# Performance work log

Measured on AMD Instinct MI355X. Metric: run time of the kernel, lower is better.

Reference implementation:

```python
import jax, jax.numpy as jnp
import numpy as np

DIM = 192
HEADS = 8
EPS = 1e-12

def conv2d(x, w, groups=1, padding='SAME'):
    return jax.lax.conv_general_dilated(
        x, w, window_strides=(1, 1), padding=padding,
        dimension_numbers=('NCHW', 'OIHW', 'NCHW'),
        feature_group_count=groups)

def setup_inputs() -> dict:
    key = jax.random.key(0)
    ks = jax.random.split(key, 6)
    b, c, h, w = 8, DIM, 128, 128
    x = jax.random.normal(ks[0], (b, c, h, w), dtype=jnp.float32)
    # depthwise 3x3 conv on x (groups=dim): OIHW with I=1
    w_dw = jax.random.normal(ks[1], (DIM, 1, 3, 3), dtype=jnp.float32) * 0.1
    # 1x1 qkv projection
    w_qkv = jax.random.normal(ks[2], (DIM * 3, DIM, 1, 1), dtype=jnp.float32) * (1.0 / np.sqrt(DIM))
    # depthwise 3x3 on qkv (groups=3*dim)
    w_qkvdw = jax.random.normal(ks[3], (DIM * 3, 1, 3, 3), dtype=jnp.float32) * 0.1
    # 1x1 output projection
    w_proj = jax.random.normal(ks[4], (DIM, DIM, 1, 1), dtype=jnp.float32) * (1.0 / np.sqrt(DIM))
    temperature = jnp.ones((HEADS, 1, 1), dtype=jnp.float32)
    rescale = jnp.ones((HEADS, 1), dtype=jnp.float32)
    return {"x": x, "w_dw": w_dw, "w_qkv": w_qkv, "w_qkvdw": w_qkvdw,
            "w_proj": w_proj, "temperature": temperature, "rescale": rescale}

def l2norm_lastdim(t):
    # matches F.normalize(t, dim=-1, eps=1e-12)
    n = jnp.sqrt(jnp.sum(t * t, axis=-1, keepdims=True))
    return t / jnp.maximum(n, EPS)

def reference(x, w_dw, w_qkv, w_qkvdw, w_proj, temperature, rescale):
    b, c, h, w = x.shape
    heads = HEADS
    c_head = c // heads
    # variance (unbiased, like torch.var default) of depthwise-conv features over H,W
    xd = conv2d(x, w_dw, groups=c)                      # [b,c,h,w]
    var = jnp.var(xd, axis=(-2, -1), ddof=1)            # [b,c]
    var = var.reshape(b, heads, c_head)                 # [b,head,c_head]
    # qkv: 1x1 conv then depthwise 3x3
    qkv = conv2d(conv2d(x, w_qkv), w_qkvdw, groups=3 * c)  # [b,3c,h,w]
    q, k, v = jnp.split(qkv, 3, axis=1)
    def to_heads(t):
        return t.reshape(b, heads, c_head, h * w)       # b head c (h w)
    q, k, v = to_heads(q), to_heads(k), to_heads(v)
    q = l2norm_lastdim(q)
    k = l2norm_lastdim(k)
    # channel attention: [b,head,c_head,c_head]
    attn = jnp.einsum('bhcn,bhdn->bhcd', q, k) * temperature
    # diagonal bias from variance, scaled per-head
    diag = rescale * var                                # [b,head,c_head]
    attn = attn + jnp.einsum('bhc,cd->bhcd', diag, jnp.eye(c_head, dtype=attn.dtype))
    attn = jax.nn.softmax(attn, axis=-1)
    out = jnp.einsum('bhcd,bhdn->bhcn', attn, v)        # [b,head,c_head,hw]
    out = out.reshape(b, c, h, w)
    return conv2d(out, w_proj)
```

## Files before the change

kernel.cpp:

```cpp
#include <hip/hip_runtime.h>
#include <hip/hip_bf16.h>

typedef unsigned short ushort_t;
typedef __bf16 bf16x8 __attribute__((ext_vector_type(8)));
typedef float f32x4 __attribute__((ext_vector_type(4)));
typedef unsigned short us8 __attribute__((ext_vector_type(8)));
typedef unsigned short us4 __attribute__((ext_vector_type(4)));

#define HW 16384
#define CDIM 192
#define QKVC 576

static __device__ __forceinline__ float b2f(unsigned short u) {
    union { unsigned int i; float f; } cv; cv.i = ((unsigned int)u) << 16; return cv.f;
}
static __device__ __forceinline__ unsigned short f2b(float f) {
    union { __bf16 h; unsigned short u; } cv; cv.h = (__bf16)f; return cv.u;
}

__global__ __launch_bounds__(256) void k_cvt(const float* __restrict__ src,
                                             ushort_t* __restrict__ dst, int n8) {
    int i = blockIdx.x * 256 + threadIdx.x;
    if (i >= n8) return;
    f32x4 a = *(const f32x4*)&src[i * 8];
    f32x4 b = *(const f32x4*)&src[i * 8 + 4];
    us8 o;
#pragma unroll
    for (int e = 0; e < 4; ++e) { o[e] = f2b(a[e]); o[4 + e] = f2b(b[e]); }
    *(us8*)&dst[i * 8] = o;
}

__global__ __launch_bounds__(256) void k_dwvar(const float* __restrict__ x,
                                               const float* __restrict__ wdw,
                                               float* __restrict__ var,
                                               ushort_t* __restrict__ xb) {
    __shared__ __align__(16) float pl[128 * 132 + 132];
    __shared__ float red[8];
    int bc = blockIdx.x;
    int c = bc % CDIM;
    const float* xp = x + (size_t)bc * HW;
    ushort_t* xbp = xb + (size_t)bc * HW;
    int t = threadIdx.x;
#pragma unroll
    for (int i = 0; i < 16; ++i) {
        int gi = t + i * 256;
        int y = gi >> 5, xq = (gi & 31) << 2;
        f32x4 v4 = *(const f32x4*)&xp[gi * 4];
        *(f32x4*)&pl[y * 132 + xq] = v4;
        us4 b4;
#pragma unroll
        for (int j = 0; j < 4; ++j) b4[j] = f2b(v4[j]);
        *(us4*)&xbp[gi * 4] = b4;
    }
    if (t < 33) { f32x4 zz = {0.f, 0.f, 0.f, 0.f}; *(f32x4*)&pl[16896 + t * 4] = zz; }
    float w[9];
#pragma unroll
    for (int j = 0; j < 9; ++j) w[j] = wdw[c * 9 + j];
    __syncthreads();

    int y = t >> 1, xs = (t & 1) * 64;
    int yb0 = (y > 0)   ? (y - 1) * 132 : 16896;
    int yb1 = y * 132;
    int yb2 = (y < 127) ? (y + 1) * 132 : 16896;
    float l0 = 0.f, l1 = 0.f, l2 = 0.f;
    if (xs != 0) { l0 = pl[yb0 + 63]; l1 = pl[yb1 + 63]; l2 = pl[yb2 + 63]; }
    float s1 = 0.f, s2 = 0.f;
#pragma unroll
    for (int g = 0; g < 8; ++g) {
        int x0 = xs + g * 8;
        float e0[10], e1[10], e2[10];
        e0[0] = l0; e1[0] = l1; e2[0] = l2;
        f32x4 a0 = *(const f32x4*)&pl[yb0 + x0], b0 = *(const f32x4*)&pl[yb0 + x0 + 4];
        f32x4 a1 = *(const f32x4*)&pl[yb1 + x0], b1 = *(const f32x4*)&pl[yb1 + x0 + 4];
        f32x4 a2 = *(const f32x4*)&pl[yb2 + x0], b2 = *(const f32x4*)&pl[yb2 + x0 + 4];
#pragma unroll
        for (int j = 0; j < 4; ++j) {
            e0[1 + j] = a0[j]; e0[5 + j] = b0[j];
            e1[1 + j] = a1[j]; e1[5 + j] = b1[j];
            e2[1 + j] = a2[j]; e2[5 + j] = b2[j];
        }
        float r0 = 0.f, r1 = 0.f, r2 = 0.f;
        if (x0 + 8 < 128) { r0 = pl[yb0 + x0 + 8]; r1 = pl[yb1 + x0 + 8]; r2 = pl[yb2 + x0 + 8]; }
        e0[9] = r0; e1[9] = r1; e2[9] = r2;
#pragma unroll
        for (int j = 0; j < 8; ++j) {
            float o = e0[j] * w[0] + e0[j + 1] * w[1] + e0[j + 2] * w[2]
                    + e1[j] * w[3] + e1[j + 1] * w[4] + e1[j + 2] * w[5]
                    + e2[j] * w[6] + e2[j + 1] * w[7] + e2[j + 2] * w[8];
            s1 += o; s2 += o * o;
        }
        l0 = e0[8]; l1 = e1[8]; l2 = e2[8];
    }
#pragma unroll
    for (int off = 32; off; off >>= 1) { s1 += __shfl_xor(s1, off); s2 += __shfl_xor(s2, off); }
    int wv = t >> 6;
    if ((t & 63) == 0) { red[wv * 2] = s1; red[wv * 2 + 1] = s2; }
    __syncthreads();
    if (t == 0) {
        float S1 = red[0] + red[2] + red[4] + red[6];
        float S2 = red[1] + red[3] + red[5] + red[7];
        var[bc] = (S2 - S1 * S1 * (1.0f / 16384.f)) * (1.0f / 16383.f);
    }
}

__global__ __launch_bounds__(256) void k_dwqkv(const ushort_t* __restrict__ qkvraw,
                                               const float* __restrict__ wqd,
                                               ushort_t* __restrict__ qkvd,
                                               float* __restrict__ ssq) {
    __shared__ __align__(16) ushort_t pl[128 * 136 + 136];
    __shared__ float red[4];
    int bo = blockIdx.x;
    int o = bo % QKVC, b = bo / QKVC;
    const ushort_t* xp = qkvraw + (size_t)bo * HW;
    ushort_t* op = qkvd + (size_t)bo * HW;
    int t = threadIdx.x;
#pragma unroll
    for (int i = 0; i < 8; ++i) {
        int gi = t + i * 256;
        int y = gi >> 4, xo = (gi & 15) * 8;
        *(us8*)&pl[y * 136 + xo] = *(const us8*)&xp[gi * 8];
    }
    if (t < 17) { us8 zz = {}; *(us8*)&pl[17408 + t * 8] = zz; }
    float w[9];
#pragma unroll
    for (int j = 0; j < 9; ++j) w[j] = wqd[o * 9 + j];
    __syncthreads();

    int y = t >> 1, xs = (t & 1) * 64;
    int yb0 = (y > 0)   ? (y - 1) * 136 : 17408;
    int yb1 = y * 136;
    int yb2 = (y < 127) ? (y + 1) * 136 : 17408;
    float l0 = 0.f, l1 = 0.f, l2 = 0.f;
    if (xs != 0) { l0 = b2f(pl[yb0 + 63]); l1 = b2f(pl[yb1 + 63]); l2 = b2f(pl[yb2 + 63]); }
    float s2 = 0.f;
#pragma unroll
    for (int g = 0; g < 8; ++g) {
        int x0 = xs + g * 8;
        us8 v0 = *(const us8*)&pl[yb0 + x0];
        us8 v1 = *(const us8*)&pl[yb1 + x0];
        us8 v2 = *(const us8*)&pl[yb2 + x0];
        float r0 = 0.f, r1 = 0.f, r2 = 0.f;
        if (x0 + 8 < 128) { r0 = b2f(pl[yb0 + x0 + 8]); r1 = b2f(pl[yb1 + x0 + 8]); r2 = b2f(pl[yb2 + x0 + 8]); }
        float e0[10], e1[10], e2[10];
        e0[0] = l0; e1[0] = l1; e2[0] = l2;
#pragma unroll
        for (int j = 0; j < 8; ++j) { e0[j + 1] = b2f(v0[j]); e1[j + 1] = b2f(v1[j]); e2[j + 1] = b2f(v2[j]); }
        e0[9] = r0; e1[9] = r1; e2[9] = r2;
        us8 ob;
#pragma unroll
        for (int j = 0; j < 8; ++j) {
            float ov = e0[j] * w[0] + e0[j + 1] * w[1] + e0[j + 2] * w[2]
                     + e1[j] * w[3] + e1[j + 1] * w[4] + e1[j + 2] * w[5]
                     + e2[j] * w[6] + e2[j + 1] * w[7] + e2[j + 2] * w[8];
            unsigned short bits = f2b(ov);
            ob[j] = bits;
            float rv = b2f(bits);
            s2 += rv * rv;
        }
        *(us8*)&op[(size_t)y * 128 + x0] = ob;
        l0 = e0[8]; l1 = e1[8]; l2 = e2[8];
    }
    if (o < 2 * CDIM) {
#pragma unroll
        for (int off = 32; off; off >>= 1) s2 += __shfl_xor(s2, off);
        int wv = t >> 6;
        if ((t & 63) == 0) red[wv] = s2;
        __syncthreads();
        if (t == 0) ssq[b * 384 + o] = red[0] + red[1] + red[2] + red[3];
    }
}

template<int CF>
__global__ __launch_bounds__(256) void k_gemm(const ushort_t* __restrict__ Av, long sAb,
                                              const ushort_t* __restrict__ Bv, long sBb,
                                              void* __restrict__ Cv, long sCb, int K) {
    __shared__ __align__(16) char smem[49152];
    ushort_t* As = (ushort_t*)smem;
    ushort_t* Bs = (ushort_t*)(smem + 24576);
    int t = threadIdx.x;
    int wv = t >> 6, lane = t & 63, quad = lane >> 4, l15 = lane & 15;
    size_t aoff = (size_t)blockIdx.z * sAb + (size_t)blockIdx.y * 192 * K;
    size_t boff = (size_t)blockIdx.z * sBb + (size_t)blockIdx.x * 128;
    size_t coff = (size_t)blockIdx.z * sCb + (size_t)blockIdx.y * 192 * HW + (size_t)blockIdx.x * 128;
    f32x4 acc[24] = {};
    int bkr = t >> 3, bn0 = (t & 7) * 16, tlow = t & 7;
    int gk0 = bkr >> 3, klo = bkr & 7;
    const ushort_t* Bp = Bv + boff;
    us8 pb0 = *(const us8*)&Bp[(size_t)bkr * HW + bn0];
    us8 pb1 = *(const us8*)&Bp[(size_t)bkr * HW + bn0 + 8];
    us8 pb2 = *(const us8*)&Bp[(size_t)(bkr + 32) * HW + bn0];
    us8 pb3 = *(const us8*)&Bp[(size_t)(bkr + 32) * HW + bn0 + 8];
    int nIter = K >> 6;
    for (int it = 0; it < nIter; ++it) {
        int kk = it << 6;
#pragma unroll
        for (int i = 0; i < 6; ++i) {
            int s = t + i * 256;
            int row = s >> 3, kc = (s & 7) * 8;
            int kcs = kc ^ ((row & 7) * 8);
            *(uint4*)&As[row * 64 + kcs] = *(const uint4*)&Av[aoff + (size_t)row * K + kk + kc];
        }
#pragma unroll
        for (int e = 0; e < 8; ++e) {
            int col0 = ((gk0 ^ tlow ^ e) << 3) + klo;
            Bs[(bn0 + e) * 64 + col0] = pb0[e];
            Bs[(bn0 + 8 + e) * 64 + col0] = pb1[e];
            int col1 = (((gk0 + 4) ^ tlow ^ e) << 3) + klo;
            Bs[(bn0 + e) * 64 + col1] = pb2[e];
            Bs[(bn0 + 8 + e) * 64 + col1] = pb3[e];
        }
        __syncthreads();
        if (it + 1 < nIter) {
            const ushort_t* Bn = &Bp[(size_t)(kk + 64) * HW];
            pb0 = *(const us8*)&Bn[(size_t)bkr * HW + bn0];
            pb1 = *(const us8*)&Bn[(size_t)bkr * HW + bn0 + 8];
            pb2 = *(const us8*)&Bn[(size_t)(bkr + 32) * HW + bn0];
            pb3 = *(const us8*)&Bn[(size_t)(bkr + 32) * HW + bn0 + 8];
        }
#pragma unroll
        for (int s = 0; s < 2; ++s) {
            int r0 = wv * 16 + l15, r1 = 64 + r0, r2 = 128 + r0;
            int ko = s * 32 + quad * 8;
            bf16x8 af0 = *(const bf16x8*)&As[r0 * 64 + (ko ^ ((r0 & 7) * 8))];
            bf16x8 af1 = *(const bf16x8*)&As[r1 * 64 + (ko ^ ((r1 & 7) * 8))];
            bf16x8 af2 = *(const bf16x8*)&As[r2 * 64 + (ko ^ ((r2 & 7) * 8))];
#pragma unroll
            for (int tc = 0; tc < 8; ++tc) {
                int n = tc * 16 + l15;
                int g = (s * 4 + quad) ^ ((tc ^ l15) & 7);
                bf16x8 bfr = *(const bf16x8*)&Bs[n * 64 + (g << 3)];
                acc[tc]      = __builtin_amdgcn_mfma_f32_16x16x32_bf16(af0, bfr, acc[tc],      0, 0, 0);
                acc[8 + tc]  = __builtin_amdgcn_mfma_f32_16x16x32_bf16(af1, bfr, acc[8 + tc],  0, 0, 0);
                acc[16 + tc] = __builtin_amdgcn_mfma_f32_16x16x32_bf16(af2, bfr, acc[16 + tc], 0, 0, 0);
            }
        }
        __syncthreads();
    }
    if (CF == 0) {
        ushort_t* Ct = (ushort_t*)smem;
#pragma unroll
        for (int rt = 0; rt < 3; ++rt)
#pragma unroll
            for (int tc = 0; tc < 8; ++tc)
#pragma unroll
                for (int r = 0; r < 4; ++r)
                    Ct[(rt * 64 + wv * 16 + quad * 4 + r) * 128 + tc * 16 + l15] = f2b(acc[rt * 8 + tc][r]);
        __syncthreads();
        ushort_t* Co = (ushort_t*)Cv;
#pragma unroll
        for (int i = 0; i < 12; ++i) {
            int s = t + i * 256;
            int row = s >> 4, c8 = (s & 15) * 8;
            *(us8*)&Co[coff + (size_t)row * HW + c8] = *(us8*)&Ct[row * 128 + c8];
        }
    } else {
        float* Cf = (float*)smem;
        float* Co = (float*)Cv;
#pragma unroll
        for (int rt = 0; rt < 3; ++rt) {
            if (rt) __syncthreads();
#pragma unroll
            for (int tc = 0; tc < 8; ++tc)
#pragma unroll
                for (int r = 0; r < 4; ++r)
                    Cf[(wv * 16 + quad * 4 + r) * 128 + tc * 16 + l15] = acc[rt * 8 + tc][r];
            __syncthreads();
#pragma unroll
            for (int i = 0; i < 8; ++i) {
                int s = t + i * 256;
                int row = s >> 5, c4 = (s & 31) * 4;
                *(f32x4*)&Co[coff + (size_t)(rt * 64 + row) * HW + c4] = *(f32x4*)&Cf[row * 128 + c4];
            }
        }
    }
}

__global__ __launch_bounds__(256) void k_gram(const ushort_t* __restrict__ qkvd,
                                              float* __restrict__ G) {
    __shared__ __align__(16) ushort_t qs[24 * 264];
    __shared__ __align__(16) ushort_t ks[24 * 264];
    int bh = blockIdx.y;
    int b = bh >> 3, h = bh & 7;
    int t = threadIdx.x, wv = t >> 6, lane = t & 63, quad = lane >> 4, l15 = lane & 15;
    const ushort_t* qb = qkvd + (size_t)b * 9437184 + (size_t)(h * 24) * HW;
    const ushort_t* kp = qb + (size_t)CDIM * HW;
    f32x4 a00 = {}, a01 = {}, a10 = {}, a11 = {};
    bf16x8 z = {};
    bool hi = (l15 < 8);
    int kbase0 = blockIdx.x * 2048;
    for (int sub = 0; sub < 8; ++sub) {
        int kbase = kbase0 + sub * 256;
#pragma unroll
        for (int j = 0; j < 3; ++j) {
            int gi = t + j * 256;
            int row = gi >> 5, c8 = (gi & 31) * 8;
            *(us8*)&qs[row * 264 + c8] = *(const us8*)&qb[(size_t)row * HW + kbase + c8];
            *(us8*)&ks[row * 264 + c8] = *(const us8*)&kp[(size_t)row * HW + kbase + c8];
        }
        __syncthreads();
#pragma unroll
        for (int s = 0; s < 2; ++s) {
            int ko = (wv * 2 + s) * 32 + quad * 8;
            bf16x8 qa0 = *(const bf16x8*)&qs[l15 * 264 + ko];
            bf16x8 qa1 = hi ? *(const bf16x8*)&qs[(16 + l15) * 264 + ko] : z;
            bf16x8 kb0 = *(const bf16x8*)&ks[l15 * 264 + ko];
            bf16x8 kb1 = hi ? *(const bf16x8*)&ks[(16 + l15) * 264 + ko] : z;
            a00 = __builtin_amdgcn_mfma_f32_16x16x32_bf16(qa0, kb0, a00, 0, 0, 0);
            a01 = __builtin_amdgcn_mfma_f32_16x16x32_bf16(qa0, kb1, a01, 0, 0, 0);
            a10 = __builtin_amdgcn_mfma_f32_16x16x32_bf16(qa1, kb0, a10, 0, 0, 0);
            a11 = __builtin_amdgcn_mfma_f32_16x16x32_bf16(qa1, kb1, a11, 0, 0, 0);
        }
        __syncthreads();
    }
    float* Gp = G + (size_t)bh * 576;
#pragma unroll
    for (int r = 0; r < 4; ++r) {
        int r0 = quad * 4 + r, r1 = 16 + quad * 4 + r;
        int c0 = l15, c1 = 16 + l15;
        atomicAdd(&Gp[r0 * 24 + c0], a00[r]);
        if (c1 < 24) atomicAdd(&Gp[r0 * 24 + c1], a01[r]);
        if (r1 < 24) atomicAdd(&Gp[r1 * 24 + c0], a10[r]);
        if (r1 < 24 && c1 < 24) atomicAdd(&Gp[r1 * 24 + c1], a11[r]);
    }
}

__global__ __launch_bounds__(256) void k_smweff(const float* __restrict__ G,
                                                const float* __restrict__ ssq,
                                                const float* __restrict__ var,
                                                const float* __restrict__ wproj,
                                                const float* __restrict__ temp,
                                                const float* __restrict__ resc,
                                                ushort_t* __restrict__ Weff) {
    int b = blockIdx.x, t = threadIdx.x;
    __shared__ float P[8 * 24 * 24];
    __shared__ float snq[192], snk[192];
    if (t < 192) {
        snq[t] = fmaxf(sqrtf(ssq[b * 384 + t]), 1e-12f);
        snk[t] = fmaxf(sqrtf(ssq[b * 384 + 192 + t]), 1e-12f);
    }
    __syncthreads();
    if (t < 192) {
        int h = t / 24, c = t % 24;
        float tmpv = temp[h];
        float dvar = resc[h] * var[b * 192 + t];
        const float* Gp = G + (size_t)(b * 8 + h) * 576 + c * 24;
        float inq = tmpv / snq[t];
        float lg[24]; float mx = -1e30f;
#pragma unroll
        for (int d = 0; d < 24; ++d) {
            float v = Gp[d] * inq / snk[h * 24 + d];
            if (d == c) v += dvar;
            lg[d] = v; mx = fmaxf(mx, v);
        }
        float sum = 0.f;
#pragma unroll
        for (int d = 0; d < 24; ++d) { float e = __expf(lg[d] - mx); lg[d] = e; sum += e; }
        float inv = 1.f / sum;
#pragma unroll
        for (int d = 0; d < 24; ++d) P[(h * 24 + c) * 24 + d] = lg[d] * inv;
    }
    __syncthreads();
#pragma unroll
    for (int i = 0; i < 6; ++i) {
        int idx = t + (blockIdx.y * 6 + i) * 256;
        int co = idx / 192, hd = idx % 192;
        int h2 = hd / 24, d = hd % 24;
        float a = 0.f;
#pragma unroll
        for (int c2 = 0; c2 < 24; ++c2)
            a += wproj[co * 192 + h2 * 24 + c2] * P[(h2 * 24 + c2) * 24 + d];
        Weff[(size_t)b * 36864 + idx] = f2b(a);
    }
}

extern "C" void kernel_launch(void* const* d_in, const int* in_sizes, int n_in,
                              void* d_out, int out_size, void* d_ws, size_t ws_size,
                              hipStream_t stream) {
    const float* x      = (const float*)d_in[0];
    const float* wdw    = (const float*)d_in[1];
    const float* wqkv   = (const float*)d_in[2];
    const float* wqkvdw = (const float*)d_in[3];
    const float* wproj  = (const float*)d_in[4];
    const float* temp   = (const float*)d_in[5];
    const float* resc   = (const float*)d_in[6];
    float* out = (float*)d_out;

    char* ws = (char*)d_ws;
    ushort_t* qkvraw = (ushort_t*)ws;
    ushort_t* qkvd   = (ushort_t*)(ws + 150994944);
    char* small = ws + 301989888;
    float* var  = (float*)small;
    float* ssq  = (float*)(small + 6144);
    float* G    = (float*)(small + 6144 + 12288);
    ushort_t* Weff = (ushort_t*)(small + 6144 + 12288 + 147456);

    ushort_t* xb  = qkvd;
    ushort_t* wqb = qkvd + 60000000;

    (void)hipMemsetAsync(G, 0, 147456, stream);
    k_cvt<<<dim3(54), dim3(256), 0, stream>>>(wqkv, wqb, 13824);
    k_dwvar<<<dim3(1536), dim3(256), 0, stream>>>(x, wdw, var, xb);
    k_gemm<0><<<dim3(128, 3, 8), dim3(256), 0, stream>>>(wqb, 0L, xb, 3145728L, qkvraw, 9437184L, 192);
    k_dwqkv<<<dim3(4608), dim3(256), 0, stream>>>(qkvraw, wqkvdw, qkvd, ssq);
    k_gram<<<dim3(8, 64), dim3(256), 0, stream>>>(qkvd, G);
    k_smweff<<<dim3(8, 24), dim3(256), 0, stream>>>(G, ssq, var, wproj, temp, resc, Weff);
    k_gemm<1><<<dim3(128, 1, 8), dim3(256), 0, stream>>>(Weff, 36864L, qkvd + (size_t)384 * HW, 9437184L, out, 3145728L, 192);
}
```

Baseline: 373.4 us.

## Split depthwise conv kernels into half-plane blocks with atomic partial reductions

Both depthwise 3x3 kernels (variance path and qkv path) now process half of a 128x128 plane per block, with halo rows loaded from the neighbouring half. This doubles the grid and roughly halves the shared memory per block, so more blocks can be resident on each CU. Partial sums are combined with atomicAdd into zeroed buffers, and the variance is finalized in the softmax kernel. The cost is extra halo loads, more atomics, and a larger memset.

```diff
diff --git a/kernel.cpp b/kernel.cpp
--- a/kernel.cpp
+++ b/kernel.cpp
@@ -32,41 +32,51 @@
 
 __global__ __launch_bounds__(256) void k_dwvar(const float* __restrict__ x,
                                                const float* __restrict__ wdw,
-                                               float* __restrict__ var,
+                                               float* __restrict__ vs1,
+                                               float* __restrict__ vs2,
                                                ushort_t* __restrict__ xb) {
-    __shared__ __align__(16) float pl[128 * 132 + 132];
+    __shared__ __align__(16) float pl[66 * 132];
     __shared__ float red[8];
-    int bc = blockIdx.x;
+    int blk = blockIdx.x;
+    int bc = blk >> 1, half = blk & 1, rb = half * 64;
     int c = bc % CDIM;
     const float* xp = x + (size_t)bc * HW;
     ushort_t* xbp = xb + (size_t)bc * HW;
     int t = threadIdx.x;
 #pragma unroll
-    for (int i = 0; i < 16; ++i) {
+    for (int i = 0; i < 8; ++i) {
         int gi = t + i * 256;
-        int y = gi >> 5, xq = (gi & 31) << 2;
-        f32x4 v4 = *(const f32x4*)&xp[gi * 4];
-        *(f32x4*)&pl[y * 132 + xq] = v4;
+        int row = gi >> 5, q4 = (gi & 31) * 4;
+        f32x4 v4 = *(const f32x4*)&xp[(size_t)(rb + row) * 128 + q4];
+        *(f32x4*)&pl[(row + 1) * 132 + q4] = v4;
         us4 b4;
 #pragma unroll
         for (int j = 0; j < 4; ++j) b4[j] = f2b(v4[j]);
-        *(us4*)&xbp[gi * 4] = b4;
-    }
-    if (t < 33) { f32x4 zz = {0.f, 0.f, 0.f, 0.f}; *(f32x4*)&pl[16896 + t * 4] = zz; }
+        *(us4*)&xbp[(size_t)(rb + row) * 128 + q4] = b4;
+    }
+    if (t < 32) {
+        f32x4 v = {0.f, 0.f, 0.f, 0.f};
+        if (rb > 0) v = *(const f32x4*)&xp[(size_t)(rb - 1) * 128 + t * 4];
+        *(f32x4*)&pl[t * 4] = v;
+    } else if (t < 64) {
+        int g = t - 32;
+        f32x4 v = {0.f, 0.f, 0.f, 0.f};
+        if (rb + 64 < 128) v = *(const f32x4*)&xp[(size_t)(rb + 64) * 128 + g * 4];
+        *(f32x4*)&pl[65 * 132 + g * 4] = v;
+    }
     float w[9];
 #pragma unroll
     for (int j = 0; j < 9; ++j) w[j] = wdw[c * 9 + j];
     __syncthreads();
 
-    int y = t >> 1, xs = (t & 1) * 64;
-    int yb0 = (y > 0)   ? (y - 1) * 132 : 16896;
-    int yb1 = y * 132;
-    int yb2 = (y < 127) ? (y + 1) * 132 : 16896;
+    int lane = t & 63, wv = t >> 6;
+    int y = lane, xs = wv * 32;
+    int yb0 = y * 132, yb1 = yb0 + 132, yb2 = yb1 + 132;
     float l0 = 0.f, l1 = 0.f, l2 = 0.f;
-    if (xs != 0) { l0 = pl[yb0 + 63]; l1 = pl[yb1 + 63]; l2 = pl[yb2 + 63]; }
+    if (xs != 0) { l0 = pl[yb0 + xs - 1]; l1 = pl[yb1 + xs - 1]; l2 = pl[yb2 + xs - 1]; }
     float s1 = 0.f, s2 = 0.f;
 #pragma unroll
-    for (int g = 0; g < 8; ++g) {
+    for (int g = 0; g < 4; ++g) {
         int x0 = xs + g * 8;
         float e0[10], e1[10], e2[10];
         e0[0] = l0; e1[0] = l1; e2[0] = l2;
@@ -79,9 +89,9 @@
             e1[1 + j] = a1[j]; e1[5 + j] = b1[j];
             e2[1 + j] = a2[j]; e2[5 + j] = b2[j];
         }
-        float r0 = 0.f, r1 = 0.f, r2 = 0.f;
-        if (x0 + 8 < 128) { r0 = pl[yb0 + x0 + 8]; r1 = pl[yb1 + x0 + 8]; r2 = pl[yb2 + x0 + 8]; }
-        e0[9] = r0; e1[9] = r1; e2[9] = r2;
+        float r0v = 0.f, r1v = 0.f, r2v = 0.f;
+        if (x0 + 8 < 128) { r0v = pl[yb0 + x0 + 8]; r1v = pl[yb1 + x0 + 8]; r2v = pl[yb2 + x0 + 8]; }
+        e0[9] = r0v; e1[9] = r1v; e2[9] = r2v;
 #pragma unroll
         for (int j = 0; j < 8; ++j) {
             float o = e0[j] * w[0] + e0[j + 1] * w[1] + e0[j + 2] * w[2]
@@ -93,13 +103,11 @@
     }
 #pragma unroll
     for (int off = 32; off; off >>= 1) { s1 += __shfl_xor(s1, off); s2 += __shfl_xor(s2, off); }
-    int wv = t >> 6;
-    if ((t & 63) == 0) { red[wv * 2] = s1; red[wv * 2 + 1] = s2; }
+    if (lane == 0) { red[wv * 2] = s1; red[wv * 2 + 1] = s2; }
     __syncthreads();
     if (t == 0) {
-        float S1 = red[0] + red[2] + red[4] + red[6];
-        float S2 = red[1] + red[3] + red[5] + red[7];
-        var[bc] = (S2 - S1 * S1 * (1.0f / 16384.f)) * (1.0f / 16383.f);
+        atomicAdd(&vs1[bc], red[0] + red[2] + red[4] + red[6]);
+        atomicAdd(&vs2[bc], red[1] + red[3] + red[5] + red[7]);
     }
 }
 
@@ -107,45 +115,54 @@
                                                const float* __restrict__ wqd,
                                                ushort_t* __restrict__ qkvd,
                                                float* __restrict__ ssq) {
-    __shared__ __align__(16) ushort_t pl[128 * 136 + 136];
+    __shared__ __align__(16) ushort_t pl[66 * 136];
     __shared__ float red[4];
-    int bo = blockIdx.x;
+    int blk = blockIdx.x;
+    int bo = blk >> 1, half = blk & 1, rb = half * 64;
     int o = bo % QKVC, b = bo / QKVC;
     const ushort_t* xp = qkvraw + (size_t)bo * HW;
     ushort_t* op = qkvd + (size_t)bo * HW;
     int t = threadIdx.x;
 #pragma unroll
-    for (int i = 0; i < 8; ++i) {
+    for (int i = 0; i < 4; ++i) {
         int gi = t + i * 256;
-        int y = gi >> 4, xo = (gi & 15) * 8;
-        *(us8*)&pl[y * 136 + xo] = *(const us8*)&xp[gi * 8];
-    }
-    if (t < 17) { us8 zz = {}; *(us8*)&pl[17408 + t * 8] = zz; }
+        int row = gi >> 4, gr = (gi & 15) * 8;
+        *(us8*)&pl[(row + 1) * 136 + gr] = *(const us8*)&xp[(size_t)(rb + row) * 128 + gr];
+    }
+    if (t < 16) {
+        us8 v = {};
+        if (rb > 0) v = *(const us8*)&xp[(size_t)(rb - 1) * 128 + t * 8];
+        *(us8*)&pl[t * 8] = v;
+    } else if (t < 32) {
+        int g = t - 16;
+        us8 v = {};
+        if (rb + 64 < 128) v = *(const us8*)&xp[(size_t)(rb + 64) * 128 + g * 8];
+        *(us8*)&pl[65 * 136 + g * 8] = v;
+    }
     float w[9];
 #pragma unroll
     for (int j = 0; j < 9; ++j) w[j] = wqd[o * 9 + j];
     __syncthreads();
 
-    int y = t >> 1, xs = (t & 1) * 64;
-    int yb0 = (y > 0)   ? (y - 1) * 136 : 17408;
-    int yb1 = y * 136;
-    int yb2 = (y < 127) ? (y + 1) * 136 : 17408;
+    int lane = t & 63, wv = t >> 6;
+    int y = lane, xs = wv * 32;
+    int yb0 = y * 136, yb1 = yb0 + 136, yb2 = yb1 + 136;
     float l0 = 0.f, l1 = 0.f, l2 = 0.f;
-    if (xs != 0) { l0 = b2f(pl[yb0 + 63]); l1 = b2f(pl[yb1 + 63]); l2 = b2f(pl[yb2 + 63]); }
+    if (xs != 0) { l0 = b2f(pl[yb0 + xs - 1]); l1 = b2f(pl[yb1 + xs - 1]); l2 = b2f(pl[yb2 + xs - 1]); }
     float s2 = 0.f;
 #pragma unroll
-    for (int g = 0; g < 8; ++g) {
+    for (int g = 0; g < 4; ++g) {
         int x0 = xs + g * 8;
         us8 v0 = *(const us8*)&pl[yb0 + x0];
         us8 v1 = *(const us8*)&pl[yb1 + x0];
         us8 v2 = *(const us8*)&pl[yb2 + x0];
-        float r0 = 0.f, r1 = 0.f, r2 = 0.f;
-        if (x0 + 8 < 128) { r0 = b2f(pl[yb0 + x0 + 8]); r1 = b2f(pl[yb1 + x0 + 8]); r2 = b2f(pl[yb2 + x0 + 8]); }
+        float r0v = 0.f, r1v = 0.f, r2v = 0.f;
+        if (x0 + 8 < 128) { r0v = b2f(pl[yb0 + x0 + 8]); r1v = b2f(pl[yb1 + x0 + 8]); r2v = b2f(pl[yb2 + x0 + 8]); }
         float e0[10], e1[10], e2[10];
         e0[0] = l0; e1[0] = l1; e2[0] = l2;
 #pragma unroll
         for (int j = 0; j < 8; ++j) { e0[j + 1] = b2f(v0[j]); e1[j + 1] = b2f(v1[j]); e2[j + 1] = b2f(v2[j]); }
-        e0[9] = r0; e1[9] = r1; e2[9] = r2;
+        e0[9] = r0v; e1[9] = r1v; e2[9] = r2v;
         us8 ob;
 #pragma unroll
         for (int j = 0; j < 8; ++j) {
@@ -157,17 +174,15 @@
             float rv = b2f(bits);
             s2 += rv * rv;
         }
-        *(us8*)&op[(size_t)y * 128 + x0] = ob;
+        *(us8*)&op[(size_t)(rb + y) * 128 + x0] = ob;
         l0 = e0[8]; l1 = e1[8]; l2 = e2[8];
     }
-    if (o < 2 * CDIM) {
-#pragma unroll
-        for (int off = 32; off; off >>= 1) s2 += __shfl_xor(s2, off);
-        int wv = t >> 6;
-        if ((t & 63) == 0) red[wv] = s2;
-        __syncthreads();
-        if (t == 0) ssq[b * 384 + o] = red[0] + red[1] + red[2] + red[3];
-    }
+#pragma unroll
+    for (int off = 32; off; off >>= 1) s2 += __shfl_xor(s2, off);
+    if (lane == 0) red[wv] = s2;
+    __syncthreads();
+    if (t == 0 && o < 2 * CDIM)
+        atomicAdd(&ssq[b * 384 + o], red[0] + red[1] + red[2] + red[3]);
 }
 
 template<int CF>
@@ -326,7 +341,8 @@
 
 __global__ __launch_bounds__(256) void k_smweff(const float* __restrict__ G,
                                                 const float* __restrict__ ssq,
-                                                const float* __restrict__ var,
+                                                const float* __restrict__ vs1,
+                                                const float* __restrict__ vs2,
                                                 const float* __restrict__ wproj,
                                                 const float* __restrict__ temp,
                                                 const float* __restrict__ resc,
@@ -342,7 +358,9 @@
     if (t < 192) {
         int h = t / 24, c = t % 24;
         float tmpv = temp[h];
-        float dvar = resc[h] * var[b * 192 + t];
+        float S1 = vs1[b * 192 + t], S2 = vs2[b * 192 + t];
+        float varv = (S2 - S1 * S1 * (1.0f / 16384.f)) * (1.0f / 16383.f);
+        float dvar = resc[h] * varv;
         const float* Gp = G + (size_t)(b * 8 + h) * 576 + c * 24;
         float inq = tmpv / snq[t];
         float lg[24]; float mx = -1e30f;
@@ -389,20 +407,21 @@
     ushort_t* qkvraw = (ushort_t*)ws;
     ushort_t* qkvd   = (ushort_t*)(ws + 150994944);
     char* small = ws + 301989888;
-    float* var  = (float*)small;
-    float* ssq  = (float*)(small + 6144);
-    float* G    = (float*)(small + 6144 + 12288);
-    ushort_t* Weff = (ushort_t*)(small + 6144 + 12288 + 147456);
+    float* vs1  = (float*)small;
+    float* vs2  = (float*)(small + 6144);
+    float* ssq  = (float*)(small + 12288);
+    float* G    = (float*)(small + 24576);
+    ushort_t* Weff = (ushort_t*)(small + 172032);
 
     ushort_t* xb  = qkvd;
     ushort_t* wqb = qkvd + 60000000;
 
-    (void)hipMemsetAsync(G, 0, 147456, stream);
+    (void)hipMemsetAsync(small, 0, 172032, stream);
     k_cvt<<<dim3(54), dim3(256), 0, stream>>>(wqkv, wqb, 13824);
-    k_dwvar<<<dim3(1536), dim3(256), 0, stream>>>(x, wdw, var, xb);
+    k_dwvar<<<dim3(3072), dim3(256), 0, stream>>>(x, wdw, vs1, vs2, xb);
     k_gemm<0><<<dim3(128, 3, 8), dim3(256), 0, stream>>>(wqb, 0L, xb, 3145728L, qkvraw, 9437184L, 192);
-    k_dwqkv<<<dim3(4608), dim3(256), 0, stream>>>(qkvraw, wqkvdw, qkvd, ssq);
+    k_dwqkv<<<dim3(9216), dim3(256), 0, stream>>>(qkvraw, wqkvdw, qkvd, ssq);
     k_gram<<<dim3(8, 64), dim3(256), 0, stream>>>(qkvd, G);
-    k_smweff<<<dim3(8, 24), dim3(256), 0, stream>>>(G, ssq, var, wproj, temp, resc, Weff);
+    k_smweff<<<dim3(8, 24), dim3(256), 0, stream>>>(G, ssq, vs1, vs2, wproj, temp, resc, Weff);
     k_gemm<1><<<dim3(128, 1, 8), dim3(256), 0, stream>>>(Weff, 36864L, qkvd + (size_t)384 * HW, 9437184L, out, 3145728L, 192);
 }
```

Measured after the change: 365.1 us. -2.2%, faster.
